# Optimization experiments

Measured on AMD Instinct MI355X. Metric: run time of the kernel, lower is better.

The kernel has to match this reference:

```python
import jax, jax.numpy as jnp
import numpy as np

B, T, H, HW = 16, 32, 512, 32  # batch, timesteps, hidden channels, spatial size


def setup_inputs() -> dict:
    key = jax.random.key(0)
    k1, k2, k3, k4, k5 = jax.random.split(key, 5)
    x = jax.random.normal(k1, (B, T, HW, HW), dtype=jnp.float32)
    # cell conv: 1x1, (1 + H) -> 4H, with bias (k=1 default, padding 'same')
    W_conv = jax.random.normal(k2, (4 * H, 1 + H, 1, 1), dtype=jnp.float32) * 0.02
    b_conv = jax.random.normal(k3, (4 * H,), dtype=jnp.float32) * 0.02
    # post conv: 3x3, H -> 1, padding 'same'
    W_post = jax.random.normal(k4, (1, H, 3, 3), dtype=jnp.float32) * 0.02
    b_post = jax.random.normal(k5, (1,), dtype=jnp.float32) * 0.02
    return {"x": x, "W_conv": W_conv, "b_conv": b_conv, "W_post": W_post, "b_post": b_post}


def _post_conv(h, W_post, b_post):
    # NCHW 3x3 'same' conv
    y = jax.lax.conv_general_dilated(
        h, W_post, window_strides=(1, 1), padding="SAME",
        dimension_numbers=("NCHW", "OIHW", "NCHW"))
    return y + b_post[None, :, None, None]


def reference(x, W_conv, b_conv, W_post, b_post):
    Wc = W_conv[:, :, 0, 0]  # [4H, 1+H] -- 1x1 conv is a channel GEMM

    def step(carry, xt):
        h, c = carry  # [B,H,32,32] each; xt [B,1,32,32]
        z = jnp.concatenate([xt, h], axis=1)  # [B,1+H,32,32]
        gates = jnp.einsum("bchw,oc->bohw", z, Wc) + b_conv[None, :, None, None]
        i, f, o, g = jnp.split(gates, 4, axis=1)
        # Faithful to source (non-standard gating):
        c = jax.nn.sigmoid(f) * c + jax.nn.sigmoid(i) + jnp.tanh(g)
        h = jax.nn.sigmoid(o) + jnp.tanh(c)
        y = _post_conv(h, W_post, b_post)  # [B,1,32,32]
        return (h, c), y

    h0 = jnp.zeros((x.shape[0], H, HW, HW), dtype=x.dtype)
    c0 = jnp.zeros_like(h0)
    xs = x[:, :, None, :, :].transpose(1, 0, 2, 3, 4)  # [T,B,1,32,32]
    _, ys = jax.lax.scan(step, (h0, c0), xs)  # ys [T,B,1,32,32]
    out = ys[:, :, 0].transpose(1, 0, 2, 3)  # [B,T,32,32] == cat along dim=1
    return out
```

## Files before the change

kernel.cpp:

```cpp
#include <hip/hip_runtime.h>
#include <cstdint>
#include <cstddef>

#define B_    16
#define T_    32
#define H_    512
#define P_    1024
#define NPOS  16384
#define NG    2048

typedef __attribute__((ext_vector_type(8))) short short8;
typedef __attribute__((ext_vector_type(4))) float f32x4;

__device__ __forceinline__ unsigned short f2bf(float f) {
  uint32_t u = __float_as_uint(f);
  u += 0x7fffu + ((u >> 16) & 1u);
  return (unsigned short)(u >> 16);
}
__device__ __forceinline__ float bflo(uint32_t u) { return __uint_as_float(u << 16); }
__device__ __forceinline__ float bfhi(uint32_t u) { return __uint_as_float(u & 0xffff0000u); }

__device__ __forceinline__ float sigf(float x) {
  return __builtin_amdgcn_rcpf(1.0f + __expf(-x));
}
__device__ __forceinline__ float tanhf_(float x) {
  return 1.0f - 2.0f * __builtin_amdgcn_rcpf(__expf(2.0f * x) + 1.0f);
}

__device__ __forceinline__ void gload_lds16(const void* g, void* l) {
  __builtin_amdgcn_global_load_lds(
      (const __attribute__((address_space(1))) void*)g,
      (__attribute__((address_space(3))) void*)l, 16, 0, 0);
}

__global__ void repack_w(const float* __restrict__ Wc, const float* __restrict__ bconv,
                         unsigned short* __restrict__ Wp, float* __restrict__ w0x,
                         float* __restrict__ bx) {
  int idx = blockIdx.x * 256 + threadIdx.x;
  int r = idx >> 9, k = idx & 511;
  int ch = r >> 2, g = r & 3;
  int o = g * 512 + ch;
  Wp[idx] = f2bf(Wc[o * 513 + 1 + k]);
  if (k == 0) { w0x[r] = Wc[o * 513]; bx[r] = bconv[o]; }
}

__global__ void repack_wpost(const float* __restrict__ Wpost, float* __restrict__ wpp) {
  int idx = blockIdx.x * 256 + threadIdx.x;
  if (idx >= 9 * 512) return;
  int j = idx >> 9, c = idx & 511;
  wpp[idx] = Wpost[c * 9 + j];
}

__global__ __launch_bounds__(256, 2)
void lstm_step(const unsigned short* __restrict__ Wp,
               const unsigned short* __restrict__ hprev,
               unsigned short* __restrict__ hnext,
               _Float16* __restrict__ Cst,
               const float* __restrict__ w0x, const float* __restrict__ bxv,
               const float* __restrict__ xin, int t) {
  __shared__ unsigned short As[256 * 64];
  __shared__ unsigned short Bs[128 * 64];

  const int tid = threadIdx.x;
  const int lane = tid & 63;
  const int wv = tid >> 6;
  const int wm = wv >> 1, wn = wv & 1;
  const int q = lane >> 4, l = lane & 15;

  const int r0 = blockIdx.x * 256;
  const int n0 = blockIdx.y * 128;

  const int srow = tid >> 3;
  const int lchunk = (tid & 7) ^ (srow & 7);
  const unsigned short* gA = Wp    + (size_t)(r0 + srow) * 512 + lchunk * 8;
  const unsigned short* gB = hprev + (size_t)(n0 + srow) * 512 + lchunk * 8;
  char* lA = (char*)As + wv * 1024;
  char* lB = (char*)Bs + wv * 1024;

  f32x4 acc[8][4] = {};

  for (int kc = 0; kc < 512; kc += 64) {
#pragma unroll
    for (int j = 0; j < 8; ++j)
      gload_lds16(gA + (size_t)j * (32 * 512) + kc, lA + j * 4096);
#pragma unroll
    for (int j = 0; j < 4; ++j)
      gload_lds16(gB + (size_t)j * (32 * 512) + kc, lB + j * 4096);
    __syncthreads();

#pragma unroll
    for (int kk = 0; kk < 2; ++kk) {
      short8 af[8], bf_[4];
#pragma unroll
      for (int mi = 0; mi < 8; ++mi) {
        int row = wm * 128 + mi * 16 + l;
        int sidx = row * 64 + (((kk * 4 + q) ^ (row & 7)) * 8);
        af[mi] = *(const short8*)(As + sidx);
      }
#pragma unroll
      for (int ni = 0; ni < 4; ++ni) {
        int row = wn * 64 + ni * 16 + l;
        int sidx = row * 64 + (((kk * 4 + q) ^ (row & 7)) * 8);
        bf_[ni] = *(const short8*)(Bs + sidx);
      }
#pragma unroll
      for (int mi = 0; mi < 8; ++mi)
#pragma unroll
        for (int ni = 0; ni < 4; ++ni)
          acc[mi][ni] = __builtin_amdgcn_mfma_f32_16x16x32_bf16(af[mi], bf_[ni], acc[mi][ni], 0, 0, 0);
    }
    __syncthreads();
  }

  float xv[4]; int posL[4]; size_t cbase[4];
#pragma unroll
  for (int ni = 0; ni < 4; ++ni) {
    posL[ni] = wn * 64 + ni * 16 + l;
    int pos = n0 + posL[ni];
    int b = pos >> 10, p = pos & 1023;
    xv[ni] = xin[((b * T_ + t) << 10) + p];
    cbase[ni] = ((size_t)b << 19) + p;
  }
  const int ch0 = blockIdx.x * 64;
#pragma unroll
  for (int mi = 0; mi < 8; ++mi) {
    int chl = wm * 32 + mi * 4 + q;
    int rg = r0 + wm * 128 + mi * 16 + q * 4;
    float4 w0 = *(const float4*)(w0x + rg);
    float4 bb = *(const float4*)(bxv + rg);
    int ch = ch0 + chl;
#pragma unroll
    for (int ni = 0; ni < 4; ++ni) {
      f32x4 g = acc[mi][ni];
      float gi = g[0] + w0.x * xv[ni] + bb.x;
      float gf = g[1] + w0.y * xv[ni] + bb.y;
      float go = g[2] + w0.z * xv[ni] + bb.z;
      float gg = g[3] + w0.w * xv[ni] + bb.w;
      size_t cidx = cbase[ni] + ((size_t)ch << 10);
      float cold = (float)Cst[cidx];
      float cn = sigf(gf) * cold + sigf(gi) + tanhf_(gg);
      float hn = sigf(go) + tanhf_(cn);
      Cst[cidx] = (_Float16)cn;
      As[posL[ni] * 64 + chl] = f2bf(hn);
    }
  }
  __syncthreads();
  {
    int pl = tid >> 1;
    int chh = (tid & 1) << 5;
    const uint4* src = (const uint4*)(As + pl * 64 + chh);
    unsigned short* dst = hnext + (size_t)(n0 + pl) * 512 + ch0 + chh;
    ((uint4*)dst)[0] = src[0];
    ((uint4*)dst)[1] = src[1];
    ((uint4*)dst)[2] = src[2];
    ((uint4*)dst)[3] = src[3];
  }
}

__global__ __launch_bounds__(256)
void post_conv(const unsigned short* __restrict__ h, const float* __restrict__ wpp,
               const float* __restrict__ bpost, float* __restrict__ out, int t) {
  int wid = blockIdx.x * 4 + (threadIdx.x >> 6);
  int lane = threadIdx.x & 63;
  int b = wid >> 10, p = wid & 1023;
  int py = p >> 5, px = p & 31;
  int c0 = lane << 3;
  float acc = 0.f;
#pragma unroll
  for (int dy = -1; dy <= 1; ++dy) {
    int ny = py + dy;
    if ((unsigned)ny > 31u) continue;
#pragma unroll
    for (int dx = -1; dx <= 1; ++dx) {
      int nx = px + dx;
      if ((unsigned)nx > 31u) continue;
      int j = (dy + 1) * 3 + (dx + 1);
      const uint4 hv = *(const uint4*)(h + ((size_t)((b << 10) + (ny << 5) + nx) << 9) + c0);
      const float4 wa = *(const float4*)(wpp + (j << 9) + c0);
      const float4 wb = *(const float4*)(wpp + (j << 9) + c0 + 4);
      acc += bflo(hv.x) * wa.x + bfhi(hv.x) * wa.y
           + bflo(hv.y) * wa.z + bfhi(hv.y) * wa.w
           + bflo(hv.z) * wb.x + bfhi(hv.z) * wb.y
           + bflo(hv.w) * wb.z + bfhi(hv.w) * wb.w;
    }
  }
#pragma unroll
  for (int off = 1; off < 64; off <<= 1)
    acc += __shfl_xor(acc, off, 64);
  if (lane == 0)
    out[((b * T_ + t) << 10) + p] = acc + bpost[0];
}

extern "C" void kernel_launch(void* const* d_in, const int* in_sizes, int n_in,
                              void* d_out, int out_size, void* d_ws, size_t ws_size,
                              hipStream_t stream) {
  const float* x     = (const float*)d_in[0];
  const float* Wconv = (const float*)d_in[1];
  const float* bconv = (const float*)d_in[2];
  const float* Wpost = (const float*)d_in[3];
  const float* bpost = (const float*)d_in[4];
  float* out = (float*)d_out;
  char* ws = (char*)d_ws;

  unsigned short* h0  = (unsigned short*)(ws);
  unsigned short* h1  = (unsigned short*)(ws + 16777216);
  _Float16*       Cst = (_Float16*)(ws + 33554432);
  unsigned short* Wp  = (unsigned short*)(ws + 50331648);
  float*          w0x = (float*)(ws + 52428800);
  float*          bx  = (float*)(ws + 52436992);
  float*          wpp = (float*)(ws + 52445184);

  hipMemsetAsync(h0, 0, 16777216, stream);
  hipMemsetAsync(Cst, 0, 16777216, stream);
  repack_w<<<4096, 256, 0, stream>>>(Wconv, bconv, Wp, w0x, bx);
  repack_wpost<<<18, 256, 0, stream>>>(Wpost, wpp);

  unsigned short* hp = h0;
  unsigned short* hn = h1;
  for (int t = 0; t < T_; ++t) {
    lstm_step<<<dim3(8, 128), 256, 0, stream>>>(Wp, hp, hn, Cst, w0x, bx, x, t);
    post_conv<<<4096, 256, 0, stream>>>(hn, wpp, bpost, out, t);
    unsigned short* tmp = hp; hp = hn; hn = tmp;
  }
}
```

Measured before the change: 2.014 ms.

## Double-buffer LDS tiles in LSTM GEMM and swizzle epilogue h staging

```diff
diff --git a/kernel.cpp b/kernel.cpp
--- a/kernel.cpp
+++ b/kernel.cpp
@@ -51,15 +51,15 @@
   wpp[idx] = Wpost[c * 9 + j];
 }
 
-__global__ __launch_bounds__(256, 2)
+__global__ __launch_bounds__(256, 1)
 void lstm_step(const unsigned short* __restrict__ Wp,
                const unsigned short* __restrict__ hprev,
                unsigned short* __restrict__ hnext,
                _Float16* __restrict__ Cst,
                const float* __restrict__ w0x, const float* __restrict__ bxv,
                const float* __restrict__ xin, int t) {
-  __shared__ unsigned short As[256 * 64];
-  __shared__ unsigned short Bs[128 * 64];
+  __shared__ unsigned short As[2][256 * 64];
+  __shared__ unsigned short Bs[2][128 * 64];
 
   const int tid = threadIdx.x;
   const int lane = tid & 63;
@@ -74,19 +74,29 @@
   const int lchunk = (tid & 7) ^ (srow & 7);
   const unsigned short* gA = Wp    + (size_t)(r0 + srow) * 512 + lchunk * 8;
   const unsigned short* gB = hprev + (size_t)(n0 + srow) * 512 + lchunk * 8;
-  char* lA = (char*)As + wv * 1024;
-  char* lB = (char*)Bs + wv * 1024;
 
   f32x4 acc[8][4] = {};
 
-  for (int kc = 0; kc < 512; kc += 64) {
+  auto stage = [&](int bb, int kc) {
+    char* lA = (char*)As[bb] + wv * 1024;
+    char* lB = (char*)Bs[bb] + wv * 1024;
 #pragma unroll
     for (int j = 0; j < 8; ++j)
       gload_lds16(gA + (size_t)j * (32 * 512) + kc, lA + j * 4096);
 #pragma unroll
     for (int j = 0; j < 4; ++j)
       gload_lds16(gB + (size_t)j * (32 * 512) + kc, lB + j * 4096);
-    __syncthreads();
+  };
+
+  stage(0, 0);
+  __syncthreads();
+
+#pragma unroll
+  for (int kt = 0; kt < 8; ++kt) {
+    const int cur = kt & 1;
+    if (kt < 7) stage(cur ^ 1, (kt + 1) * 64);
+    const unsigned short* Ab = As[cur];
+    const unsigned short* Bb = Bs[cur];
 
 #pragma unroll
     for (int kk = 0; kk < 2; ++kk) {
@@ -95,13 +105,13 @@
       for (int mi = 0; mi < 8; ++mi) {
         int row = wm * 128 + mi * 16 + l;
         int sidx = row * 64 + (((kk * 4 + q) ^ (row & 7)) * 8);
-        af[mi] = *(const short8*)(As + sidx);
+        af[mi] = *(const short8*)(Ab + sidx);
       }
 #pragma unroll
       for (int ni = 0; ni < 4; ++ni) {
         int row = wn * 64 + ni * 16 + l;
         int sidx = row * 64 + (((kk * 4 + q) ^ (row & 7)) * 8);
-        bf_[ni] = *(const short8*)(Bs + sidx);
+        bf_[ni] = *(const short8*)(Bb + sidx);
       }
 #pragma unroll
       for (int mi = 0; mi < 8; ++mi)
@@ -141,19 +151,18 @@
       float cn = sigf(gf) * cold + sigf(gi) + tanhf_(gg);
       float hn = sigf(go) + tanhf_(cn);
       Cst[cidx] = (_Float16)cn;
-      As[posL[ni] * 64 + chl] = f2bf(hn);
+      As[0][posL[ni] * 64 + (chl ^ ((posL[ni] & 7) << 3))] = f2bf(hn);
     }
   }
   __syncthreads();
   {
     int pl = tid >> 1;
-    int chh = (tid & 1) << 5;
-    const uint4* src = (const uint4*)(As + pl * 64 + chh);
-    unsigned short* dst = hnext + (size_t)(n0 + pl) * 512 + ch0 + chh;
-    ((uint4*)dst)[0] = src[0];
-    ((uint4*)dst)[1] = src[1];
-    ((uint4*)dst)[2] = src[2];
-    ((uint4*)dst)[3] = src[3];
+    int cb = (tid & 1) << 2;
+    const unsigned short* srcrow = As[0] + pl * 64;
+    unsigned short* dst = hnext + (size_t)(n0 + pl) * 512 + ch0 + (cb << 3);
+#pragma unroll
+    for (int i = 0; i < 4; ++i)
+      ((uint4*)dst)[i] = *(const uint4*)(srcrow + (((cb + i) ^ (pl & 7)) << 3));
   }
 }
 
```

Result: slower. 2.803 ms (+39.2%).
